# Kernel tuning notes

Hardware: AMD Instinct MI355X
Metric: run time of the kernel (lower is better)

## Reference

```python
import jax, jax.numpy as jnp
import numpy as np

EMBED = 256      # embedding_dim
HEADS = 4        # attn_heads
OUT = EMBED // HEADS  # out_channels per head = 64
R = 8            # n_relations = len(metapaths) + 1
N = 16384        # num_nodes
NEG_SLOPE = 0.2  # PyG GATv2 default leaky_relu slope


def setup_inputs() -> dict:
    key = jax.random.key(0)
    ks = jax.random.split(key, 16)
    s = 0.05
    inp = {"relation_embs": jax.random.normal(ks[0], (N, R, EMBED), jnp.float32)}
    # Two GATv2Conv layers: lin_l (src), lin_r (dst), att vector, output bias.
    for i in range(2):
        inp[f"Wl{i}"] = jax.random.normal(ks[1 + 6 * i], (EMBED, HEADS, OUT), jnp.float32) * s
        inp[f"bl{i}"] = jax.random.normal(ks[2 + 6 * i], (HEADS, OUT), jnp.float32) * s
        inp[f"Wr{i}"] = jax.random.normal(ks[3 + 6 * i], (EMBED, HEADS, OUT), jnp.float32) * s
        inp[f"br{i}"] = jax.random.normal(ks[4 + 6 * i], (HEADS, OUT), jnp.float32) * s
        inp[f"att{i}"] = jax.random.normal(ks[5 + 6 * i], (HEADS, OUT), jnp.float32) * s
        inp[f"bias{i}"] = jax.random.normal(ks[6 + 6 * i], (HEADS * OUT,), jnp.float32) * s
    return inp


def reference(relation_embs, Wl0, bl0, Wr0, br0, att0, bias0,
              Wl1, bl1, Wr1, br1, att1, bias1):
    # Each node owns a fully-connected graph over its R relation embeddings
    # (all rows nonzero under randn fill), so the PyG gather/softmax/scatter
    # collapses to dense [N, R_dst, R_src] attention.
    h = jax.nn.relu(relation_embs)                                  # [N,R,D]

    # ---- GATv2 layer 0: full FC edges (every src -> every dst) ----
    xl = jnp.einsum('nrd,dhc->nrhc', h, Wl0) + bl0                  # src feats [N,R,H,C]
    xr = jnp.einsum('nrd,dhc->nrhc', h, Wr0) + br0                  # dst feats [N,R,H,C]
    e = jax.nn.leaky_relu(xr[:, :, None] + xl[:, None], NEG_SLOPE)  # [N,Ri,Rj,H,C]
    logits = jnp.einsum('nijhc,hc->nijh', e, att0)                  # [N,Ri,Rj,H]
    alpha = jax.nn.softmax(logits, axis=2)                          # softmax over src j
    h = jnp.einsum('nijh,njhc->nihc', alpha, xl)                    # [N,R,H,C]
    h = h.reshape(N, R, HEADS * OUT) + bias0
    h = jax.nn.relu(h)

    # ---- GATv2 layer 1 (last): only edges into the self node (nid == R-1) ----
    xl = jnp.einsum('nrd,dhc->nrhc', h, Wl1) + bl1                  # src feats [N,R,H,C]
    xr_self = jnp.einsum('nd,dhc->nhc', h[:, -1], Wr1) + br1        # dst = self [N,H,C]
    e = jax.nn.leaky_relu(xr_self[:, None] + xl, NEG_SLOPE)         # [N,R,H,C]
    logits = jnp.einsum('nrhc,hc->nrh', e, att1)                    # [N,R,H]
    alpha = jax.nn.softmax(logits, axis=1)                          # softmax over src r
    out = jnp.einsum('nrh,nrhc->nhc', alpha, xl).reshape(N, HEADS * OUT) + bias1
    node_embs = jax.nn.relu(out)                                    # [N, D]

    # betas: last-layer attention into the self node, detached (SparseTensor.to_dense().detach())
    betas = jax.lax.stop_gradient(alpha)                            # [N,R,H]
    return node_embs, betas
```

## Files before the change

### kernel.cpp

```cpp
#include <hip/hip_runtime.h>


#define NNODES 16384
#define NB 8
#define MR 64

typedef _Float16 f16x8 __attribute__((ext_vector_type(8)));
typedef _Float16 f16x4 __attribute__((ext_vector_type(4)));
typedef _Float16 f16x2 __attribute__((ext_vector_type(2)));
typedef float f32x4 __attribute__((ext_vector_type(4)));

#if __has_builtin(__builtin_amdgcn_fdot2)
#define FDOT2(a, b, c) __builtin_amdgcn_fdot2((a), (b), (c), false)
#else
#define FDOT2(a, b, c) ((c) + (float)(a)[0] * (float)(b)[0] + (float)(a)[1] * (float)(b)[1])
#endif

__device__ __forceinline__ f16x2 pk2(float a, float b) {
    return __builtin_bit_cast(f16x2, __builtin_amdgcn_cvt_pkrtz(a, b));
}

__device__ __forceinline__ f16x2 leaky2(f16x2 t) {
#if __has_builtin(__builtin_elementwise_max)
    return __builtin_elementwise_max(t, t * (f16x2){(_Float16)0.2f, (_Float16)0.2f});
#else
    const unsigned u = __builtin_bit_cast(unsigned, t) & 0x7FFF7FFFu;
    const f16x2 at = __builtin_bit_cast(f16x2, u);
    return t * (f16x2){(_Float16)0.6f, (_Float16)0.6f} +
           at * (f16x2){(_Float16)0.4f, (_Float16)0.4f};
#endif
}
__device__ __forceinline__ f16x2 relu2(f16x2 t) {
#if __has_builtin(__builtin_elementwise_max)
    return __builtin_elementwise_max(t, (f16x2){(_Float16)0.f, (_Float16)0.f});
#else
    const unsigned u = __builtin_bit_cast(unsigned, t) & 0x7FFF7FFFu;
    const f16x2 at = __builtin_bit_cast(f16x2, u);
    return (t + at) * (f16x2){(_Float16)0.5f, (_Float16)0.5f};
#endif
}

__device__ __forceinline__ int swz(int row, int chunk) {
    return row * 256 + ((chunk ^ (row & 7)) << 3);
}
__device__ __forceinline__ int cswz(int row, int col) {
    return row * 128 + (((col >> 3) ^ (row & 7)) << 3) + (col & 7);
}

__global__ void prep_weights(const float* __restrict__ Wl0, const float* __restrict__ Wr0,
                             const float* __restrict__ Wl1, const float* __restrict__ Wr1,
                             _Float16* __restrict__ wt) {
    __shared__ float tile[64 * 68];
    const int t  = threadIdx.x;
    const int m  = blockIdx.x >> 4;
    const int kt = (blockIdx.x >> 2) & 3;
    const int nt = blockIdx.x & 3;
    const float* src = (m == 0 ? Wl0 : m == 1 ? Wr0 : m == 2 ? Wl1 : Wr1) + kt * 64 * 256;
    #pragma unroll
    for (int i = 0; i < 4; ++i) {
        const int idx = i * 256 + t;
        const int kk  = idx >> 4;
        const int nn  = (idx & 15) * 4;
        const float4 v = *(const float4*)&src[kk * 256 + nt * 64 + nn];
        tile[kk * 68 + nn + 0] = v.x;
        tile[kk * 68 + nn + 1] = v.y;
        tile[kk * 68 + nn + 2] = v.z;
        tile[kk * 68 + nn + 3] = v.w;
    }
    __syncthreads();
    const int n  = t >> 2;
    const int ks = (t & 3) * 16;
    f16x8 o0, o1;
    #pragma unroll
    for (int e = 0; e < 8; ++e) o0[e] = (_Float16)tile[(ks + e) * 68 + n];
    #pragma unroll
    for (int e = 0; e < 8; ++e) o1[e] = (_Float16)tile[(ks + 8 + e) * 68 + n];
    _Float16* dst = &wt[(size_t)(m * 256 + nt * 64 + n) * 256 + kt * 64 + ks];
    *(f16x8*)dst = o0;
    *(f16x8*)(dst + 8) = o1;
}

__launch_bounds__(512, 4)
__global__ void gemm0(const float* __restrict__ x,
                      const float* __restrict__ bl0, const float* __restrict__ br0,
                      const _Float16* __restrict__ wt,
                      _Float16* __restrict__ X1) {
    __shared__ _Float16 A[128 * 256];
    __shared__ _Float16 Cb[64 * 128];
    const int mb   = blockIdx.x;
    const int row0 = mb * 128;
    const int tid  = threadIdx.x;
    const int lane = tid & 63;
    const int wv   = tid >> 6;
    const int lr   = lane & 15;
    const int lq   = lane >> 4;
    const int wr   = wv >> 2;
    const int wc   = wv & 3;

    {
        const float4* src = (const float4*)(x + (size_t)row0 * 256);
        #pragma unroll
        for (int it = 0; it < 8; ++it) {
            const int g = it * 512 + tid;
            const int row = g >> 5, c = g & 31;
            const float4 v0 = src[2 * g];
            const float4 v1 = src[2 * g + 1];
            f16x8 s;
            s[0] = (_Float16)fmaxf(v0.x, 0.f); s[1] = (_Float16)fmaxf(v0.y, 0.f);
            s[2] = (_Float16)fmaxf(v0.z, 0.f); s[3] = (_Float16)fmaxf(v0.w, 0.f);
            s[4] = (_Float16)fmaxf(v1.x, 0.f); s[5] = (_Float16)fmaxf(v1.y, 0.f);
            s[6] = (_Float16)fmaxf(v1.z, 0.f); s[7] = (_Float16)fmaxf(v1.w, 0.f);
            *(f16x8*)&A[swz(row, c)] = s;
        }
    }
    __syncthreads();

    for (int nq = 0; nq < 4; ++nq) {
        f32x4 acc[4][2];
        #pragma unroll
        for (int m = 0; m < 4; ++m)
            #pragma unroll
            for (int n = 0; n < 2; ++n)
                acc[m][n] = f32x4{0.f, 0.f, 0.f, 0.f};
        const _Float16* wq = wt + (size_t)(nq * 128 + wc * 32) * 256;
        f16x8 b[2][2];
        b[0][0] = *(const f16x8*)&wq[(size_t)lr * 256 + lq * 8];
        b[0][1] = *(const f16x8*)&wq[(size_t)(16 + lr) * 256 + lq * 8];
        #pragma unroll
        for (int kt = 0; kt < 8; ++kt) {
            const int cur = kt & 1, nxt = cur ^ 1;
            if (kt < 7) {
                const int koff = (kt + 1) * 32 + lq * 8;
                b[nxt][0] = *(const f16x8*)&wq[(size_t)lr * 256 + koff];
                b[nxt][1] = *(const f16x8*)&wq[(size_t)(16 + lr) * 256 + koff];
            }
            f16x8 a[4];
            #pragma unroll
            for (int m = 0; m < 4; ++m)
                a[m] = *(const f16x8*)&A[swz(wr * 64 + m * 16 + lr, kt * 4 + lq)];
            #pragma unroll
            for (int m = 0; m < 4; ++m)
                #pragma unroll
                for (int n = 0; n < 2; ++n)
                    acc[m][n] = __builtin_amdgcn_mfma_f32_16x16x32_f16(a[m], b[cur][n], acc[m][n], 0, 0, 0);
        }
        #pragma unroll
        for (int mh = 0; mh < 2; ++mh) {
            __syncthreads();
            if (wr == mh) {
                #pragma unroll
                for (int n = 0; n < 2; ++n) {
                    const int col  = wc * 32 + n * 16 + lr;
                    const int gcol = nq * 128 + col;
                    const float bias = (gcol < 256) ? bl0[gcol] : br0[gcol - 256];
                    #pragma unroll
                    for (int m = 0; m < 4; ++m)
                        #pragma unroll
                        for (int r = 0; r < 4; ++r) {
                            const int row = m * 16 + lq * 4 + r;
                            Cb[cswz(row, col)] = (_Float16)(acc[m][n][r] + bias);
                        }
                }
            }
            __syncthreads();
            #pragma unroll
            for (int it = 0; it < 2; ++it) {
                const int g = it * 512 + tid;
                const int row = g >> 4, ch = g & 15;
                const f16x8 v = *(const f16x8*)&Cb[row * 128 + ((ch ^ (row & 7)) << 3)];
                *(f16x8*)&X1[(size_t)(row0 + mh * 64 + row) * 512 + nq * 128 + ch * 8] = v;
            }
        }
    }
}

__launch_bounds__(512, 4)
__global__ void gat_attn(const float* __restrict__ att0, const float* __restrict__ bias0,
                         const float* __restrict__ bl1, const float* __restrict__ br1,
                         const float* __restrict__ att1, const float* __restrict__ bias1,
                         const _Float16* __restrict__ wt,
                         const _Float16* __restrict__ X1,
                         float* __restrict__ out) {
    __shared__ _Float16 bufA[MR * 256];
    __shared__ _Float16 bufB[MR * 256];
    __shared__ float attbuf[2304];
    __shared__ _Float16 attH[768];

    const int tid  = threadIdx.x;
    const int bg   = blockIdx.x;
    const int lane = tid & 63;
    const int wv   = tid >> 6;
    const int lr   = lane & 15;
    const int lq   = lane >> 4;

    {
        const _Float16* src = X1 + (size_t)bg * 64 * 512;
        #pragma unroll
        for (int it = 0; it < 4; ++it) {
            const int g = it * 512 + tid;
            const int row = g >> 5, c = g & 31;
            const f16x8 vl = *(const f16x8*)&src[(size_t)row * 512 + c * 8];
            const f16x8 vr = *(const f16x8*)&src[(size_t)row * 512 + 256 + c * 8];
            *(f16x8*)&bufB[swz(row, c)] = vl;
            *(f16x8*)&bufA[swz(row, c)] = vr;
        }
        if (tid < 256) {
            attH[tid]       = (_Float16)att0[tid];
            attH[512 + tid] = (_Float16)bias0[tid];
        } else {
            attH[tid]       = (_Float16)att1[tid - 256];
        }
    }
    __syncthreads();

    {
        const int n  = tid >> 6;
        const int i  = (tid >> 3) & 7;
        const int h  = (tid >> 1) & 3;
        const int jh = tid & 1;
        const int rowR = n * 8 + i;
        f16x2 xr2[32];
        #pragma unroll
        for (int cc = 0; cc < 8; ++cc) {
            const int c3 = (cc + 2 * h) & 7;
            const f16x8 v = *(const f16x8*)&bufA[swz(rowR, h * 8 + c3)];
            xr2[cc * 4 + 0] = f16x2{v[0], v[1]};
            xr2[cc * 4 + 1] = f16x2{v[2], v[3]};
            xr2[cc * 4 + 2] = f16x2{v[4], v[5]};
            xr2[cc * 4 + 3] = f16x2{v[6], v[7]};
        }
        f16x8 lbuf[2][4];
        f16x8 abuf[2];
        {
            const int c3 = (2 * h) & 7;
            abuf[0] = *(const f16x8*)&attH[h * 64 + c3 * 8];
            #pragma unroll
            for (int jj = 0; jj < 4; ++jj)
                lbuf[0][jj] = *(const f16x8*)&bufB[swz(n * 8 + jh * 4 + jj, h * 8 + c3)];
        }
        float lg[4] = {0.f, 0.f, 0.f, 0.f};
        #pragma unroll
        for (int cc = 0; cc < 8; ++cc) {
            const int cur = cc & 1, nxt = cur ^ 1;
            if (cc < 7) {
                const int c3n = (cc + 1 + 2 * h) & 7;
                abuf[nxt] = *(const f16x8*)&attH[h * 64 + c3n * 8];
                #pragma unroll
                for (int jj = 0; jj < 4; ++jj)
                    lbuf[nxt][jj] = *(const f16x8*)&bufB[swz(n * 8 + jh * 4 + jj, h * 8 + c3n)];
            }
            const f16x8 a8 = abuf[cur];
            const f16x2 a2[4] = {{a8[0], a8[1]}, {a8[2], a8[3]}, {a8[4], a8[5]}, {a8[6], a8[7]}};
            #pragma unroll
            for (int jj = 0; jj < 4; ++jj) {
                const f16x8 l8 = lbuf[cur][jj];
                const f16x2 l2[4] = {{l8[0], l8[1]}, {l8[2], l8[3]}, {l8[4], l8[5]}, {l8[6], l8[7]}};
                #pragma unroll
                for (int p = 0; p < 4; ++p) {
                    const f16x2 t = leaky2(xr2[cc * 4 + p] + l2[p]);
                    lg[jj] = FDOT2(t, a2[p], lg[jj]);
                }
            }
        }
        float mx = fmaxf(fmaxf(lg[0], lg[1]), fmaxf(lg[2], lg[3]));
        mx = fmaxf(mx, __shfl_xor(mx, 1));
        float ex[4], ssum = 0.f;
        #pragma unroll
        for (int jj = 0; jj < 4; ++jj) { ex[jj] = __expf(lg[jj] - mx); ssum += ex[jj]; }
        const float tot = ssum + __shfl_xor(ssum, 1);
        const float inv = 1.f / tot;
        #pragma unroll
        for (int jj = 0; jj < 4; ++jj)
            attbuf[((n * 8 + i) * 4 + h) * 8 + jh * 4 + jj] = ex[jj] * inv;
    }
    __syncthreads();

    {
        const int row  = tid >> 3;
        const int sub  = tid & 7;
        const int h    = sub >> 1;
        const int half = sub & 1;
        const int nn   = row >> 3;
        const int cb   = h * 8 + half * 4;
        _Float16 ahv[8];
        #pragma unroll
        for (int j = 0; j < 8; ++j) ahv[j] = (_Float16)attbuf[(row * 4 + h) * 8 + j];
        f16x2 acc2[16];
        #pragma unroll
        for (int p = 0; p < 16; ++p) acc2[p] = (f16x2){(_Float16)0.f, (_Float16)0.f};
        f16x8 vbuf[2][4];
        #pragma unroll
        for (int cc = 0; cc < 4; ++cc)
            vbuf[0][cc] = *(const f16x8*)&bufB[swz(nn * 8, cb + ((cc + h) & 3))];
        #pragma unroll
        for (int j = 0; j < 8; ++j) {
            const int cur = j & 1, nxt = cur ^ 1;
            if (j < 7) {
                #pragma unroll
                for (int cc = 0; cc < 4; ++cc)
                    vbuf[nxt][cc] = *(const f16x8*)&bufB[swz(nn * 8 + j + 1, cb + ((cc + h) & 3))];
            }
            const f16x2 a2 = {ahv[j], ahv[j]};
            #pragma unroll
            for (int cc = 0; cc < 4; ++cc) {
                const f16x8 v = vbuf[cur][cc];
                acc2[cc * 4 + 0] += f16x2{v[0], v[1]} * a2;
                acc2[cc * 4 + 1] += f16x2{v[2], v[3]} * a2;
                acc2[cc * 4 + 2] += f16x2{v[4], v[5]} * a2;
                acc2[cc * 4 + 3] += f16x2{v[6], v[7]} * a2;
            }
        }
        #pragma unroll
        for (int cc = 0; cc < 4; ++cc) {
            const int c = cb + ((cc + h) & 3);
            const f16x8 b8 = *(const f16x8*)&attH[512 + c * 8];
            f16x8 s;
            #pragma unroll
            for (int p = 0; p < 4; ++p) {
                const f16x2 r = relu2(acc2[cc * 4 + p] + f16x2{b8[2 * p], b8[2 * p + 1]});
                s[2 * p]     = r[0];
                s[2 * p + 1] = r[1];
            }
            *(f16x8*)&bufA[swz(row, c)] = s;
        }
    }
    __syncthreads();

    {
        f32x4 accl[4][2], accr[2];
        #pragma unroll
        for (int m = 0; m < 4; ++m)
            #pragma unroll
            for (int n = 0; n < 2; ++n)
                accl[m][n] = f32x4{0.f, 0.f, 0.f, 0.f};
        #pragma unroll
        for (int n = 0; n < 2; ++n) accr[n] = f32x4{0.f, 0.f, 0.f, 0.f};
        const _Float16* W1l = wt + 512 * 256;
        const _Float16* W1r = wt + 768 * 256;
        const int rowS = (lr & 7) * 8 + 7;
        #pragma unroll
        for (int kt = 0; kt < 8; ++kt) {
            const int koff = kt * 32 + lq * 8;
            f16x8 a[4], as, bl[2], br[2];
            #pragma unroll
            for (int m = 0; m < 4; ++m)
                a[m] = *(const f16x8*)&bufA[swz(m * 16 + lr, kt * 4 + lq)];
            as = *(const f16x8*)&bufA[swz(rowS, kt * 4 + lq)];
            #pragma unroll
            for (int n = 0; n < 2; ++n) {
                bl[n] = *(const f16x8*)&W1l[(size_t)(wv * 32 + n * 16 + lr) * 256 + koff];
                br[n] = *(const f16x8*)&W1r[(size_t)(wv * 32 + n * 16 + lr) * 256 + koff];
            }
            #pragma unroll
            for (int m = 0; m < 4; ++m)
                #pragma unroll
                for (int n = 0; n < 2; ++n)
                    accl[m][n] = __builtin_amdgcn_mfma_f32_16x16x32_f16(a[m], bl[n], accl[m][n], 0, 0, 0);
            #pragma unroll
            for (int n = 0; n < 2; ++n)
                accr[n] = __builtin_amdgcn_mfma_f32_16x16x32_f16(as, br[n], accr[n], 0, 0, 0);
        }
        #pragma unroll
        for (int n = 0; n < 2; ++n) {
            const int col = wv * 32 + n * 16 + lr;
            const float b1 = bl1[col], b2 = br1[col];
            const int ch = col >> 3, ce = col & 7;
            #pragma unroll
            for (int m = 0; m < 4; ++m)
                #pragma unroll
                for (int r = 0; r < 4; ++r) {
                    const int row = m * 16 + lq * 4 + r;
                    bufB[swz(row, ch) + ce] = (_Float16)(accl[m][n][r] + b1);
                }
            if (lq < 2) {
                #pragma unroll
                for (int r = 0; r < 4; ++r) {
                    const int node = lq * 4 + r;
                    attbuf[node * 256 + col] = accr[n][r] + b2;
                }
            }
        }
    }
    __syncthreads();

    {
        const int n  = tid >> 5;
        const int rr = (tid >> 2) & 7;
        const int h  = tid & 3;
        float lg = 0.f;
        if (tid < 256) {
            const int rowj = n * 8 + rr;
            float4 xbuf0[2], xbuf1[2];
            f16x8 lbuf[2], abuf[2];
            {
                const int c = h * 8 + ((2 * h) & 7);
                xbuf0[0] = *(const float4*)&attbuf[n * 256 + c * 8];
                xbuf1[0] = *(const float4*)&attbuf[n * 256 + c * 8 + 4];
                lbuf[0]  = *(const f16x8*)&bufB[swz(rowj, c)];
                abuf[0]  = *(const f16x8*)&attH[256 + c * 8];
            }
            #pragma unroll
            for (int cc = 0; cc < 8; ++cc) {
                const int cur = cc & 1, nxt = cur ^ 1;
                if (cc < 7) {
                    const int cn = h * 8 + ((cc + 1 + 2 * h) & 7);
                    xbuf0[nxt] = *(const float4*)&attbuf[n * 256 + cn * 8];
                    xbuf1[nxt] = *(const float4*)&attbuf[n * 256 + cn * 8 + 4];
                    lbuf[nxt]  = *(const f16x8*)&bufB[swz(rowj, cn)];
                    abuf[nxt]  = *(const f16x8*)&attH[256 + cn * 8];
                }
                const float4 r0 = xbuf0[cur], r1 = xbuf1[cur];
                const f16x2 x2[4] = {pk2(r0.x, r0.y), pk2(r0.z, r0.w),
                                     pk2(r1.x, r1.y), pk2(r1.z, r1.w)};
                const f16x8 l8 = lbuf[cur];
                const f16x2 l2[4] = {{l8[0], l8[1]}, {l8[2], l8[3]}, {l8[4], l8[5]}, {l8[6], l8[7]}};
                const f16x8 a8 = abuf[cur];
                const f16x2 a2[4] = {{a8[0], a8[1]}, {a8[2], a8[3]}, {a8[4], a8[5]}, {a8[6], a8[7]}};
                #pragma unroll
                for (int p = 0; p < 4; ++p) {
                    const f16x2 t = leaky2(x2[p] + l2[p]);
                    lg = FDOT2(t, a2[p], lg);
                }
            }
        }
        __syncthreads();
        if (tid < 256) attbuf[2048 + tid] = lg;
        __syncthreads();
        if (tid < 256) {
            float M = -1e30f;
            float l[8];
            #pragma unroll
            for (int j = 0; j < 8; ++j) {
                l[j] = attbuf[2048 + n * 32 + j * 4 + h];
                M = fmaxf(M, l[j]);
            }
            float S = 0.f;
            #pragma unroll
            for (int j = 0; j < 8; ++j) S += __expf(l[j] - M);
            const float a = __expf(lg - M) / S;
            attbuf[tid] = a;
            out[(size_t)NNODES * 256 + (size_t)(bg * NB + n) * 32 + rr * 4 + h] = a;
        }
    }
    __syncthreads();

    {
        const int n  = tid >> 6;
        const int q  = tid & 63;
        const int c0 = q * 4;
        const int h  = q >> 4;
        f16x4 v[8];
        float a[8];
        #pragma unroll
        for (int r = 0; r < 8; ++r) {
            v[r] = *(const f16x4*)&bufB[swz(n * 8 + r, q >> 1) + (q & 1) * 4];
            a[r] = attbuf[n * 32 + r * 4 + h];
        }
        float o0 = 0.f, o1 = 0.f, o2 = 0.f, o3 = 0.f;
        #pragma unroll
        for (int r = 0; r < 8; ++r) {
            o0 = fmaf((float)v[r][0], a[r], o0);
            o1 = fmaf((float)v[r][1], a[r], o1);
            o2 = fmaf((float)v[r][2], a[r], o2);
            o3 = fmaf((float)v[r][3], a[r], o3);
        }
        float4 res;
        res.x = fmaxf(o0 + bias1[c0 + 0], 0.f);
        res.y = fmaxf(o1 + bias1[c0 + 1], 0.f);
        res.z = fmaxf(o2 + bias1[c0 + 2], 0.f);
        res.w = fmaxf(o3 + bias1[c0 + 3], 0.f);
        *(float4*)&out[(size_t)(bg * NB + n) * 256 + c0] = res;
    }
}

__launch_bounds__(512, 4)
__global__ void gat_fused(const float* __restrict__ x,
                          const float* __restrict__ bl0, const float* __restrict__ br0,
                          const float* __restrict__ att0, const float* __restrict__ bias0,
                          const float* __restrict__ bl1, const float* __restrict__ br1,
                          const float* __restrict__ att1, const float* __restrict__ bias1,
                          const _Float16* __restrict__ wt,
                          float* __restrict__ out) {
    __shared__ _Float16 bufA[MR * 256];
    __shared__ _Float16 bufB[MR * 256];
    __shared__ float attbuf[2304];
    __shared__ _Float16 attH[768];

    const int tid  = threadIdx.x;
    const int bg   = blockIdx.x;
    const int lane = tid & 63;
    const int wv   = tid >> 6;
    const int lr   = lane & 15;
    const int lq   = lane >> 4;

    {
        const float4* src = (const float4*)(x + (size_t)bg * (MR * 256));
        #pragma unroll
        for (int it = 0; it < 4; ++it) {
            const int g   = it * 512 + tid;
            const int row = g >> 5;
            const int c   = g & 31;
            const float4 v0 = src[2 * g];
            const float4 v1 = src[2 * g + 1];
            f16x8 s;
            s[0] = (_Float16)fmaxf(v0.x, 0.f); s[1] = (_Float16)fmaxf(v0.y, 0.f);
            s[2] = (_Float16)fmaxf(v0.z, 0.f); s[3] = (_Float16)fmaxf(v0.w, 0.f);
            s[4] = (_Float16)fmaxf(v1.x, 0.f); s[5] = (_Float16)fmaxf(v1.y, 0.f);
            s[6] = (_Float16)fmaxf(v1.z, 0.f); s[7] = (_Float16)fmaxf(v1.w, 0.f);
            *(f16x8*)&bufA[swz(row, c)] = s;
        }
        if (tid < 256) {
            attH[tid]       = (_Float16)att0[tid];
            attH[512 + tid] = (_Float16)bias0[tid];
        } else {
            attH[tid]       = (_Float16)att1[tid - 256];
        }
    }
    __syncthreads();

    {
        f32x4 acc[4][4];
        #pragma unroll
        for (int m = 0; m < 4; ++m)
            #pragma unroll
            for (int n = 0; n < 4; ++n)
                acc[m][n] = f32x4{0.f, 0.f, 0.f, 0.f};
        #pragma unroll
        for (int kt = 0; kt < 8; ++kt) {
            f16x8 a[4], b[4];
            #pragma unroll
            for (int m = 0; m < 4; ++m)
                a[m] = *(const f16x8*)&bufA[swz(m * 16 + lr, kt * 4 + lq)];
            const int koff = kt * 32 + lq * 8;
            #pragma unroll
            for (int n = 0; n < 4; ++n)
                b[n] = *(const f16x8*)&wt[(size_t)(wv * 64 + n * 16 + lr) * 256 + koff];
            #pragma unroll
            for (int m = 0; m < 4; ++m)
                #pragma unroll
                for (int n = 0; n < 4; ++n)
                    acc[m][n] = __builtin_amdgcn_mfma_f32_16x16x32_f16(a[m], b[n], acc[m][n], 0, 0, 0);
        }
        __syncthreads();
        _Float16* dstbuf = (wv < 4) ? bufB : bufA;
        const float* bv = (wv < 4) ? bl0 : br0;
        #pragma unroll
        for (int n = 0; n < 4; ++n) {
            const int cl   = (wv & 3) * 64 + n * 16 + lr;
            const float bias = bv[cl];
            const int ch   = cl >> 3, ce = cl & 7;
            #pragma unroll
            for (int m = 0; m < 4; ++m)
                #pragma unroll
                for (int r = 0; r < 4; ++r) {
                    const int row = m * 16 + lq * 4 + r;
                    dstbuf[swz(row, ch) + ce] = (_Float16)(acc[m][n][r] + bias);
                }
        }
    }
    __syncthreads();

    {
        const int n  = tid >> 6;
        const int i  = (tid >> 3) & 7;
        const int h  = (tid >> 1) & 3;
        const int jh = tid & 1;
        const int rowR = n * 8 + i;
        f16x2 xr2[32];
        #pragma unroll
        for (int cc = 0; cc < 8; ++cc) {
            const int c3 = (cc + 2 * h) & 7;
            const f16x8 v = *(const f16x8*)&bufA[swz(rowR, h * 8 + c3)];
            xr2[cc * 4 + 0] = f16x2{v[0], v[1]};
            xr2[cc * 4 + 1] = f16x2{v[2], v[3]};
            xr2[cc * 4 + 2] = f16x2{v[4], v[5]};
            xr2[cc * 4 + 3] = f16x2{v[6], v[7]};
        }
        f16x8 lbuf[2][4];
        f16x8 abuf[2];
        {
            const int c3 = (2 * h) & 7;
            abuf[0] = *(const f16x8*)&attH[h * 64 + c3 * 8];
            #pragma unroll
            for (int jj = 0; jj < 4; ++jj)
                lbuf[0][jj] = *(const f16x8*)&bufB[swz(n * 8 + jh * 4 + jj, h * 8 + c3)];
        }
        float lg[4] = {0.f, 0.f, 0.f, 0.f};
        #pragma unroll
        for (int cc = 0; cc < 8; ++cc) {
            const int cur = cc & 1, nxt = cur ^ 1;
            if (cc < 7) {
                const int c3n = (cc + 1 + 2 * h) & 7;
                abuf[nxt] = *(const f16x8*)&attH[h * 64 + c3n * 8];
                #pragma unroll
                for (int jj = 0; jj < 4; ++jj)
                    lbuf[nxt][jj] = *(const f16x8*)&bufB[swz(n * 8 + jh * 4 + jj, h * 8 + c3n)];
            }
            const f16x8 a8 = abuf[cur];
            const f16x2 a2[4] = {{a8[0], a8[1]}, {a8[2], a8[3]}, {a8[4], a8[5]}, {a8[6], a8[7]}};
            #pragma unroll
            for (int jj = 0; jj < 4; ++jj) {
                const f16x8 l8 = lbuf[cur][jj];
                const f16x2 l2[4] = {{l8[0], l8[1]}, {l8[2], l8[3]}, {l8[4], l8[5]}, {l8[6], l8[7]}};
                #pragma unroll
                for (int p = 0; p < 4; ++p) {
                    const f16x2 t = leaky2(xr2[cc * 4 + p] + l2[p]);
                    lg[jj] = FDOT2(t, a2[p], lg[jj]);
                }
            }
        }
        float mx = fmaxf(fmaxf(lg[0], lg[1]), fmaxf(lg[2], lg[3]));
        mx = fmaxf(mx, __shfl_xor(mx, 1));
        float ex[4], ssum = 0.f;
        #pragma unroll
        for (int jj = 0; jj < 4; ++jj) { ex[jj] = __expf(lg[jj] - mx); ssum += ex[jj]; }
        const float tot = ssum + __shfl_xor(ssum, 1);
        const float inv = 1.f / tot;
        #pragma unroll
        for (int jj = 0; jj < 4; ++jj)
            attbuf[((n * 8 + i) * 4 + h) * 8 + jh * 4 + jj] = ex[jj] * inv;
    }
    __syncthreads();

    {
        const int row  = tid >> 3;
        const int sub  = tid & 7;
        const int h    = sub >> 1;
        const int half = sub & 1;
        const int nn   = row >> 3;
        const int cb   = h * 8 + half * 4;
        _Float16 ahv[8];
        #pragma unroll
        for (int j = 0; j < 8; ++j) ahv[j] = (_Float16)attbuf[(row * 4 + h) * 8 + j];
        f16x2 acc2[16];
        #pragma unroll
        for (int p = 0; p < 16; ++p) acc2[p] = (f16x2){(_Float16)0.f, (_Float16)0.f};
        f16x8 vbuf[2][4];
        #pragma unroll
        for (int cc = 0; cc < 4; ++cc)
            vbuf[0][cc] = *(const f16x8*)&bufB[swz(nn * 8, cb + ((cc + h) & 3))];
        #pragma unroll
        for (int j = 0; j < 8; ++j) {
            const int cur = j & 1, nxt = cur ^ 1;
            if (j < 7) {
                #pragma unroll
                for (int cc = 0; cc < 4; ++cc)
                    vbuf[nxt][cc] = *(const f16x8*)&bufB[swz(nn * 8 + j + 1, cb + ((cc + h) & 3))];
            }
            const f16x2 a2 = {ahv[j], ahv[j]};
            #pragma unroll
            for (int cc = 0; cc < 4; ++cc) {
                const f16x8 v = vbuf[cur][cc];
                acc2[cc * 4 + 0] += f16x2{v[0], v[1]} * a2;
                acc2[cc * 4 + 1] += f16x2{v[2], v[3]} * a2;
                acc2[cc * 4 + 2] += f16x2{v[4], v[5]} * a2;
                acc2[cc * 4 + 3] += f16x2{v[6], v[7]} * a2;
            }
        }
        #pragma unroll
        for (int cc = 0; cc < 4; ++cc) {
            const int c = cb + ((cc + h) & 3);
            const f16x8 b8 = *(const f16x8*)&attH[512 + c * 8];
            f16x8 s;
            #pragma unroll
            for (int p = 0; p < 4; ++p) {
                const f16x2 r = relu2(acc2[cc * 4 + p] + f16x2{b8[2 * p], b8[2 * p + 1]});
                s[2 * p]     = r[0];
                s[2 * p + 1] = r[1];
            }
            *(f16x8*)&bufA[swz(row, c)] = s;
        }
    }
    __syncthreads();

    {
        f32x4 accl[4][2], accr[2];
        #pragma unroll
        for (int m = 0; m < 4; ++m)
            #pragma unroll
            for (int n = 0; n < 2; ++n)
                accl[m][n] = f32x4{0.f, 0.f, 0.f, 0.f};
        #pragma unroll
        for (int n = 0; n < 2; ++n) accr[n] = f32x4{0.f, 0.f, 0.f, 0.f};
        const _Float16* W1l = wt + 512 * 256;
        const _Float16* W1r = wt + 768 * 256;
        const int rowS = (lr & 7) * 8 + 7;
        #pragma unroll
        for (int kt = 0; kt < 8; ++kt) {
            const int koff = kt * 32 + lq * 8;
            f16x8 a[4], as, bl[2], br[2];
            #pragma unroll
            for (int m = 0; m < 4; ++m)
                a[m] = *(const f16x8*)&bufA[swz(m * 16 + lr, kt * 4 + lq)];
            as = *(const f16x8*)&bufA[swz(rowS, kt * 4 + lq)];
            #pragma unroll
            for (int n = 0; n < 2; ++n) {
                bl[n] = *(const f16x8*)&W1l[(size_t)(wv * 32 + n * 16 + lr) * 256 + koff];
                br[n] = *(const f16x8*)&W1r[(size_t)(wv * 32 + n * 16 + lr) * 256 + koff];
            }
            #pragma unroll
            for (int m = 0; m < 4; ++m)
                #pragma unroll
                for (int n = 0; n < 2; ++n)
                    accl[m][n] = __builtin_amdgcn_mfma_f32_16x16x32_f16(a[m], bl[n], accl[m][n], 0, 0, 0);
            #pragma unroll
            for (int n = 0; n < 2; ++n)
                accr[n] = __builtin_amdgcn_mfma_f32_16x16x32_f16(as, br[n], accr[n], 0, 0, 0);
        }
        #pragma unroll
        for (int n = 0; n < 2; ++n) {
            const int col = wv * 32 + n * 16 + lr;
            const float b1 = bl1[col], b2 = br1[col];
            const int ch = col >> 3, ce = col & 7;
            #pragma unroll
            for (int m = 0; m < 4; ++m)
                #pragma unroll
                for (int r = 0; r < 4; ++r) {
                    const int row = m * 16 + lq * 4 + r;
                    bufB[swz(row, ch) + ce] = (_Float16)(accl[m][n][r] + b1);
                }
            if (lq < 2) {
                #pragma unroll
                for (int r = 0; r < 4; ++r) {
                    const int node = lq * 4 + r;
                    attbuf[node * 256 + col] = accr[n][r] + b2;
                }
            }
        }
    }
    __syncthreads();

    {
        const int n  = tid >> 5;
        const int rr = (tid >> 2) & 7;
        const int h  = tid & 3;
        float lg = 0.f;
        if (tid < 256) {
            const int rowj = n * 8 + rr;
            float4 xbuf0[2], xbuf1[2];
            f16x8 lbuf[2], abuf[2];
            {
                const int c = h * 8 + ((2 * h) & 7);
                xbuf0[0] = *(const float4*)&attbuf[n * 256 + c * 8];
                xbuf1[0] = *(const float4*)&attbuf[n * 256 + c * 8 + 4];
                lbuf[0]  = *(const f16x8*)&bufB[swz(rowj, c)];
                abuf[0]  = *(const f16x8*)&attH[256 + c * 8];
            }
            #pragma unroll
            for (int cc = 0; cc < 8; ++cc) {
                const int cur = cc & 1, nxt = cur ^ 1;
                if (cc < 7) {
                    const int cn = h * 8 + ((cc + 1 + 2 * h) & 7);
                    xbuf0[nxt] = *(const float4*)&attbuf[n * 256 + cn * 8];
                    xbuf1[nxt] = *(const float4*)&attbuf[n * 256 + cn * 8 + 4];
                    lbuf[nxt]  = *(const f16x8*)&bufB[swz(rowj, cn)];
                    abuf[nxt]  = *(const f16x8*)&attH[256 + cn * 8];
                }
                const float4 r0 = xbuf0[cur], r1 = xbuf1[cur];
                const f16x2 x2[4] = {pk2(r0.x, r0.y), pk2(r0.z, r0.w),
                                     pk2(r1.x, r1.y), pk2(r1.z, r1.w)};
                const f16x8 l8 = lbuf[cur];
                const f16x2 l2[4] = {{l8[0], l8[1]}, {l8[2], l8[3]}, {l8[4], l8[5]}, {l8[6], l8[7]}};
                const f16x8 a8 = abuf[cur];
                const f16x2 a2[4] = {{a8[0], a8[1]}, {a8[2], a8[3]}, {a8[4], a8[5]}, {a8[6], a8[7]}};
                #pragma unroll
                for (int p = 0; p < 4; ++p) {
                    const f16x2 t = leaky2(x2[p] + l2[p]);
                    lg = FDOT2(t, a2[p], lg);
                }
            }
        }
        __syncthreads();
        if (tid < 256) attbuf[2048 + tid] = lg;
        __syncthreads();
        if (tid < 256) {
            float M = -1e30f;
            float l[8];
            #pragma unroll
            for (int j = 0; j < 8; ++j) {
                l[j] = attbuf[2048 + n * 32 + j * 4 + h];
                M = fmaxf(M, l[j]);
            }
            float S = 0.f;
            #pragma unroll
            for (int j = 0; j < 8; ++j) S += __expf(l[j] - M);
            const float a = __expf(lg - M) / S;
            attbuf[tid] = a;
            out[(size_t)NNODES * 256 + (size_t)(bg * NB + n) * 32 + rr * 4 + h] = a;
        }
    }
    __syncthreads();

    {
        const int n  = tid >> 6;
        const int q  = tid & 63;
        const int c0 = q * 4;
        const int h  = q >> 4;
        f16x4 v[8];
        float a[8];
        #pragma unroll
        for (int r = 0; r < 8; ++r) {
            v[r] = *(const f16x4*)&bufB[swz(n * 8 + r, q >> 1) + (q & 1) * 4];
            a[r] = attbuf[n * 32 + r * 4 + h];
        }
        float o0 = 0.f, o1 = 0.f, o2 = 0.f, o3 = 0.f;
        #pragma unroll
        for (int r = 0; r < 8; ++r) {
            o0 = fmaf((float)v[r][0], a[r], o0);
            o1 = fmaf((float)v[r][1], a[r], o1);
            o2 = fmaf((float)v[r][2], a[r], o2);
            o3 = fmaf((float)v[r][3], a[r], o3);
        }
        float4 res;
        res.x = fmaxf(o0 + bias1[c0 + 0], 0.f);
        res.y = fmaxf(o1 + bias1[c0 + 1], 0.f);
        res.z = fmaxf(o2 + bias1[c0 + 2], 0.f);
        res.w = fmaxf(o3 + bias1[c0 + 3], 0.f);
        *(float4*)&out[(size_t)(bg * NB + n) * 256 + c0] = res;
    }
}

extern "C" void kernel_launch(void* const* d_in, const int* in_sizes, int n_in,
                              void* d_out, int out_size, void* d_ws, size_t ws_size,
                              hipStream_t stream) {
    const float* x     = (const float*)d_in[0];
    const float* Wl0   = (const float*)d_in[1];
    const float* bl0   = (const float*)d_in[2];
    const float* Wr0   = (const float*)d_in[3];
    const float* br0   = (const float*)d_in[4];
    const float* att0  = (const float*)d_in[5];
    const float* bias0 = (const float*)d_in[6];
    const float* Wl1   = (const float*)d_in[7];
    const float* bl1   = (const float*)d_in[8];
    const float* Wr1   = (const float*)d_in[9];
    const float* br1   = (const float*)d_in[10];
    const float* att1  = (const float*)d_in[11];
    const float* bias1 = (const float*)d_in[12];
    _Float16* wt = (_Float16*)d_ws;
    float* out = (float*)d_out;

    prep_weights<<<64, 256, 0, stream>>>(Wl0, Wr0, Wl1, Wr1, wt);

    const size_t X1_off  = 524288;
    const size_t X1_size = (size_t)131072 * 512 * 2;
    if (ws_size >= X1_off + X1_size) {
        _Float16* X1 = (_Float16*)((char*)d_ws + X1_off);
        gemm0<<<1024, 512, 0, stream>>>(x, bl0, br0, wt, X1);
        gat_attn<<<NNODES / NB, 512, 0, stream>>>(att0, bias0, bl1, br1,
                                                  att1, bias1, wt, X1, out);
    } else {
        gat_fused<<<NNODES / NB, 512, 0, stream>>>(x, bl0, br0, att0, bias0,
                                                   bl1, br1, att1, bias1, wt, out);
    }
}
```

Baseline: 374.0 us.

## Store gemm0 output in MFMA fragment layout and scatter it in attention kernel

gemm0 no longer stages its accumulator tile through shared memory with two block barriers. Each wave now writes its MFMA fragments straight to global memory in a fragment-native blocked layout, using contiguous 8-byte stores per lane. gat_attn reads this blocked layout with f16x4 loads and scatters the elements into its swizzled shared buffers with scalar 2-byte LDS stores. The change also frees 16KB of LDS in gemm0 and reshapes its inner loop to load each A fragment just before use. The cost is that the layout transpose moves into the attention kernel as many small LDS writes, which may cause bank conflicts.

```diff
diff --git a/kernel.cpp b/kernel.cpp
--- a/kernel.cpp
+++ b/kernel.cpp
@@ -43,9 +43,6 @@
 __device__ __forceinline__ int swz(int row, int chunk) {
     return row * 256 + ((chunk ^ (row & 7)) << 3);
 }
-__device__ __forceinline__ int cswz(int row, int col) {
-    return row * 128 + (((col >> 3) ^ (row & 7)) << 3) + (col & 7);
-}
 
 __global__ void prep_weights(const float* __restrict__ Wl0, const float* __restrict__ Wr0,
                              const float* __restrict__ Wl1, const float* __restrict__ Wr1,
@@ -86,7 +83,6 @@
                       const _Float16* __restrict__ wt,
                       _Float16* __restrict__ X1) {
     __shared__ _Float16 A[128 * 256];
-    __shared__ _Float16 Cb[64 * 128];
     const int mb   = blockIdx.x;
     const int row0 = mb * 128;
     const int tid  = threadIdx.x;
@@ -134,41 +130,25 @@
                 b[nxt][0] = *(const f16x8*)&wq[(size_t)lr * 256 + koff];
                 b[nxt][1] = *(const f16x8*)&wq[(size_t)(16 + lr) * 256 + koff];
             }
-            f16x8 a[4];
-            #pragma unroll
-            for (int m = 0; m < 4; ++m)
-                a[m] = *(const f16x8*)&A[swz(wr * 64 + m * 16 + lr, kt * 4 + lq)];
-            #pragma unroll
-            for (int m = 0; m < 4; ++m)
+            #pragma unroll
+            for (int m = 0; m < 4; ++m) {
+                const f16x8 a = *(const f16x8*)&A[swz(wr * 64 + m * 16 + lr, kt * 4 + lq)];
                 #pragma unroll
                 for (int n = 0; n < 2; ++n)
-                    acc[m][n] = __builtin_amdgcn_mfma_f32_16x16x32_f16(a[m], b[cur][n], acc[m][n], 0, 0, 0);
-        }
-        #pragma unroll
-        for (int mh = 0; mh < 2; ++mh) {
-            __syncthreads();
-            if (wr == mh) {
-                #pragma unroll
-                for (int n = 0; n < 2; ++n) {
-                    const int col  = wc * 32 + n * 16 + lr;
-                    const int gcol = nq * 128 + col;
-                    const float bias = (gcol < 256) ? bl0[gcol] : br0[gcol - 256];
-                    #pragma unroll
-                    for (int m = 0; m < 4; ++m)
-                        #pragma unroll
-                        for (int r = 0; r < 4; ++r) {
-                            const int row = m * 16 + lq * 4 + r;
-                            Cb[cswz(row, col)] = (_Float16)(acc[m][n][r] + bias);
-                        }
-                }
-            }
-            __syncthreads();
-            #pragma unroll
-            for (int it = 0; it < 2; ++it) {
-                const int g = it * 512 + tid;
-                const int row = g >> 4, ch = g & 15;
-                const f16x8 v = *(const f16x8*)&Cb[row * 128 + ((ch ^ (row & 7)) << 3)];
-                *(f16x8*)&X1[(size_t)(row0 + mh * 64 + row) * 512 + nq * 128 + ch * 8] = v;
+                    acc[m][n] = __builtin_amdgcn_mfma_f32_16x16x32_f16(a, b[cur][n], acc[m][n], 0, 0, 0);
+            }
+        }
+        const size_t sbase = (((size_t)(mb * 2 + wr) * 4 + nq) * 4 + wc) * (8 * 256);
+        #pragma unroll
+        for (int n = 0; n < 2; ++n) {
+            const int gcol = nq * 128 + wc * 32 + n * 16 + lr;
+            const float bias = (gcol < 256) ? bl0[gcol] : br0[gcol - 256];
+            #pragma unroll
+            for (int m = 0; m < 4; ++m) {
+                f16x4 v;
+                #pragma unroll
+                for (int r = 0; r < 4; ++r) v[r] = (_Float16)(acc[m][n][r] + bias);
+                *(f16x4*)&X1[sbase + (size_t)(m * 2 + n) * 256 + lane * 4] = v;
             }
         }
     }
@@ -194,15 +174,24 @@
     const int lq   = lane >> 4;
 
     {
-        const _Float16* src = X1 + (size_t)bg * 64 * 512;
-        #pragma unroll
-        for (int it = 0; it < 4; ++it) {
-            const int g = it * 512 + tid;
-            const int row = g >> 5, c = g & 31;
-            const f16x8 vl = *(const f16x8*)&src[(size_t)row * 512 + c * 8];
-            const f16x8 vr = *(const f16x8*)&src[(size_t)row * 512 + 256 + c * 8];
-            *(f16x8*)&bufB[swz(row, c)] = vl;
-            *(f16x8*)&bufA[swz(row, c)] = vr;
+        const _Float16* src = X1 + (size_t)bg * 32768;
+        #pragma unroll
+        for (int i = 0; i < 16; ++i) {
+            const int flat  = i * 512 + tid;
+            const int lane_s = flat & 63;
+            const int mn  = (flat >> 6) & 7;
+            const int wcq = (flat >> 9) & 3;
+            const int nq  = flat >> 11;
+            const int m = mn >> 1, n = mn & 1;
+            const int lqs = lane_s >> 4, lrs = lane_s & 15;
+            const f16x4 v = *(const f16x4*)&src[(((size_t)nq * 4 + wcq) * 8 + mn) * 256 + lane_s * 4];
+            const int col = nq * 128 + wcq * 32 + n * 16 + lrs;
+            _Float16* dst = (col < 256) ? bufB : bufA;
+            const int cc = (col & 255) >> 3, ce = col & 7;
+            const int rbase = m * 16 + lqs * 4;
+            #pragma unroll
+            for (int r = 0; r < 4; ++r)
+                dst[swz(rbase + r, cc) + ce] = v[r];
         }
         if (tid < 256) {
             attH[tid]       = (_Float16)att0[tid];
```

Result: faster. 366.6 us (-2.0%).
